# Kernel tuning notes

Measured on AMD Instinct MI355X. Metric: run time of the kernel, lower is better.

Reference implementation:

```python
import jax, jax.numpy as jnp
import numpy as np

EPS_LN = 1e-5
EPS_ATTN = 1e-8
NUM_ITER = 3

B, N, DIN = 64, 4096, 256
K, D, H = 8, 256, 512


def layer_norm(x, g, b):
    m = jnp.mean(x, axis=-1, keepdims=True)
    v = jnp.mean((x - m) ** 2, axis=-1, keepdims=True)
    return (x - m) * jax.lax.rsqrt(v + EPS_LN) * g + b


def gru_cell(x, h, W_ih, b_ih, W_hh, b_hh):
    # torch GRUCell: gates ordered (reset, update, new)
    gi = x @ W_ih.T + b_ih  # [BK, 3D]
    gh = h @ W_hh.T + b_hh
    ir, iz, inn = jnp.split(gi, 3, axis=-1)
    hr, hz, hn = jnp.split(gh, 3, axis=-1)
    r = jax.nn.sigmoid(ir + hr)
    z = jax.nn.sigmoid(iz + hz)
    n = jnp.tanh(inn + r * hn)
    return (1.0 - z) * n + z * h


def setup_inputs() -> dict:
    key = jax.random.key(0)
    ks = jax.random.split(key, 16)
    s = 1.0 / np.sqrt(D)
    si = 1.0 / np.sqrt(DIN)
    inp = {
        'inputs': jax.random.normal(ks[0], (B, N, DIN), jnp.float32),
        'noise': jax.random.normal(ks[1], (B, K, D), jnp.float32),
        'slot_mu': jax.random.normal(ks[2], (1, 1, D), jnp.float32),
        'slot_log_sigma': jnp.zeros((1, 1, D), jnp.float32),
        'Wq': jax.random.uniform(ks[3], (D, D), jnp.float32, -s, s),
        'bq': jnp.zeros((D,), jnp.float32),
        'Wk': jax.random.uniform(ks[4], (D, DIN), jnp.float32, -si, si),
        'bk': jnp.zeros((D,), jnp.float32),
        'Wv': jax.random.uniform(ks[5], (D, DIN), jnp.float32, -si, si),
        'bv': jnp.zeros((D,), jnp.float32),
        'W_ih': jax.random.uniform(ks[6], (3 * D, D), jnp.float32, -s, s),
        'b_ih': jnp.zeros((3 * D,), jnp.float32),
        'W_hh': jax.random.uniform(ks[7], (3 * D, D), jnp.float32, -s, s),
        'b_hh': jnp.zeros((3 * D,), jnp.float32),
        'ln_in_g': jnp.ones((DIN,), jnp.float32), 'ln_in_b': jnp.zeros((DIN,), jnp.float32),
        'ln_s_g': jnp.ones((D,), jnp.float32), 'ln_s_b': jnp.zeros((D,), jnp.float32),
        'ln_ff_g': jnp.ones((D,), jnp.float32), 'ln_ff_b': jnp.zeros((D,), jnp.float32),
        'W1': jax.random.uniform(ks[8], (H, D), jnp.float32, -s, s),
        'b1': jnp.zeros((H,), jnp.float32),
        'W2': jax.random.uniform(ks[9], (D, H), jnp.float32, -1.0 / np.sqrt(H), 1.0 / np.sqrt(H)),
        'b2': jnp.zeros((D,), jnp.float32),
    }
    return inp


def reference(inputs, noise, slot_mu, slot_log_sigma, Wq, bq, Wk, bk, Wv, bv,
              W_ih, b_ih, W_hh, b_hh, ln_in_g, ln_in_b, ln_s_g, ln_s_b,
              ln_ff_g, ln_ff_b, W1, b1, W2, b2):
    scale = D ** -0.5
    slots = slot_mu + jnp.exp(slot_log_sigma) * noise  # [B,K,D]
    x = layer_norm(inputs, ln_in_g, ln_in_b)
    k = x @ Wk.T + bk  # [B,N,D]
    v = x @ Wv.T + bv  # [B,N,D]
    attn = None
    for _ in range(NUM_ITER):
        slots_prev = slots
        sn = layer_norm(slots, ln_s_g, ln_s_b)
        q = sn @ Wq.T + bq  # [B,K,D]
        dots = jnp.einsum('bkd,bnd->bkn', q, k) * scale
        attn = jax.nn.softmax(dots, axis=1)  # softmax over slots
        attn_norm = attn / (jnp.sum(attn, axis=-1, keepdims=True) + EPS_ATTN)
        updates = jnp.einsum('bkn,bnd->bkd', attn_norm, v)
        h = gru_cell(updates.reshape(-1, D), slots_prev.reshape(-1, D),
                     W_ih, b_ih, W_hh, b_hh).reshape(slots.shape)
        ff = layer_norm(h, ln_ff_g, ln_ff_b)
        slots = h + (jax.nn.relu(ff @ W1.T + b1) @ W2.T + b2)
    return slots, attn
```

## Files before the change

### kernel.cpp

```cpp
#include <hip/hip_runtime.h>
#include <hip/hip_bf16.h>
#include <math.h>

typedef __bf16 bf16x8 __attribute__((ext_vector_type(8)));
typedef float f32x4 __attribute__((ext_vector_type(4)));

#define DEV static __device__ __forceinline__

DEV unsigned short f2b(float f){
  unsigned int u = __float_as_uint(f);
  u += 0x7fffu + ((u>>16)&1u);
  return (unsigned short)(u>>16);
}
DEV float b2f(unsigned short h){ return __uint_as_float(((unsigned int)h)<<16); }
DEV unsigned int pck(float a, float b){
  return (unsigned int)f2b(a) | ((unsigned int)f2b(b)<<16);
}
DEV f32x4 mfma16(bf16x8 a, bf16x8 b, f32x4 c){
  return __builtin_amdgcn_mfma_f32_16x16x32_bf16(a,b,c,0,0,0);
}
DEV float sigm(float x){ return 1.f/(1.f+expf(-x)); }

__global__ __launch_bounds__(256) void k_slots_init(
    const float* __restrict__ noise, const float* __restrict__ mu,
    const float* __restrict__ ls, float* __restrict__ sf,
    unsigned short* __restrict__ sb){
  int i = blockIdx.x*256 + threadIdx.x;
  int d = i & 255;
  float val = mu[d] + expf(ls[d]) * noise[i];
  sf[i] = val; sb[i] = f2b(val);
}

__global__ __launch_bounds__(256) void k_prep_b16(
    const float* __restrict__ Whh, const float* __restrict__ W1,
    const float* __restrict__ W2,
    unsigned short* __restrict__ Whhb, unsigned short* __restrict__ W1b,
    unsigned short* __restrict__ W2b){
  int i = blockIdx.x*256 + threadIdx.x;
  if (i < 196608) Whhb[i] = f2b(Whh[i]);
  else if (i < 327680) W1b[i-196608] = f2b(W1[i-196608]);
  else if (i < 458752) W2b[i-327680] = f2b(W2[i-327680]);
}

__global__ __launch_bounds__(256) void k_pre1(
    const float* __restrict__ Wq, const float* __restrict__ Wk,
    const float* __restrict__ bq, const float* __restrict__ bk,
    unsigned short* __restrict__ WcT, float* __restrict__ bc,
    float* __restrict__ wqbk, float* __restrict__ cbk){
  int c = blockIdx.x, d = threadIdx.x;
  float acc = 0.f;
  for (int e=0;e<256;e++)
    acc += Wq[e*256+d] * Wk[e*256+c];
  WcT[c*256+d] = f2b(acc);
  __shared__ float red[256];
  red[d] = bq[d] * Wk[d*256+c];
  __syncthreads();
  for (int s2=128;s2>0;s2>>=1){ if (d<s2) red[d]+=red[d+s2]; __syncthreads(); }
  if (d==0) bc[c] = red[0];
  if (blockIdx.x==0){
    float a2=0.f;
    for (int e=0;e<256;e++) a2 += Wq[e*256+d]*bk[e];
    wqbk[d] = a2;
    __syncthreads();
    red[d] = bq[d]*bk[d];
    __syncthreads();
    for (int s2=128;s2>0;s2>>=1){ if (d<s2) red[d]+=red[d+s2]; __syncthreads(); }
    if (d==0) cbk[0] = red[0];
  }
}

__global__ __launch_bounds__(256) void k_pre2(
    const float* __restrict__ W_ih, const float* __restrict__ Wv,
    const float* __restrict__ bv, const float* __restrict__ b_ih,
    unsigned short* __restrict__ WvihT, float* __restrict__ bvih){
  int j = blockIdx.x, c = threadIdx.x;
  float acc=0.f;
  for (int d=0; d<256; d++)
    acc += W_ih[j*256+d] * Wv[d*256+c];
  WvihT[j*256+c] = f2b(acc);
  __shared__ float red[256];
  red[c] = bv[c] * W_ih[j*256+c];
  __syncthreads();
  for (int s2=128;s2>0;s2>>=1){ if (c<s2) red[c]+=red[c+s2]; __syncthreads(); }
  if (c==0) bvih[j] = red[0] + b_ih[j];
}

__global__ __launch_bounds__(256) void k_slot_q(
    const float* __restrict__ sf, const float* __restrict__ g,
    const float* __restrict__ be,
    const unsigned short* __restrict__ WcT, const float* __restrict__ bc,
    const float* __restrict__ wqbk, const float* __restrict__ cbk,
    unsigned short* __restrict__ qp, float* __restrict__ dotbias,
    float* __restrict__ attn_sum){
  __shared__ __align__(16) unsigned short sn[16][264];
  int b = blockIdx.x, t = threadIdx.x;
  if (t < 8) attn_sum[b*8+t] = 0.f;
  if (t < 8) dotbias[b*16+8+t] = 0.f;
  int r = t>>5, j = t&31;
  const float* pr = sf + (b*8+r)*256 + j*8;
  float v[8]; float s=0.f;
  #pragma unroll
  for (int i=0;i<8;i++){ v[i]=pr[i]; s+=v[i]; }
  s += __shfl_xor(s,1); s+=__shfl_xor(s,2); s+=__shfl_xor(s,4);
  s += __shfl_xor(s,8); s+=__shfl_xor(s,16);
  float m = s*(1.f/256.f);
  float vs=0.f;
  #pragma unroll
  for (int i=0;i<8;i++){ float d = v[i]-m; vs += d*d; }
  vs += __shfl_xor(vs,1); vs+=__shfl_xor(vs,2); vs+=__shfl_xor(vs,4);
  vs += __shfl_xor(vs,8); vs+=__shfl_xor(vs,16);
  float rstd = rsqrtf(vs*(1.f/256.f) + 1e-5f);
  float dp = 0.f;
  #pragma unroll
  for (int i=0;i<8;i++){
    int d = j*8+i;
    float snv = (v[i]-m)*rstd*g[d] + be[d];
    sn[r][d] = f2b(snv);
    dp += snv * wqbk[d];
  }
  dp += __shfl_xor(dp,1); dp+=__shfl_xor(dp,2); dp+=__shfl_xor(dp,4);
  dp += __shfl_xor(dp,8); dp+=__shfl_xor(dp,16);
  if (j==0) dotbias[b*16+r] = dp + cbk[0];
  for (int rr=8; rr<16; ++rr){ sn[rr][t]=0; if (t<8) sn[rr][256+t]=0; }
  __syncthreads();
  int lane = t&63, wv = t>>6, l16 = lane&15, quad = lane>>4;
  #pragma unroll
  for (int nt=0; nt<4; ++nt){
    int col = (wv*4+nt)*16 + l16;
    f32x4 acc = {0.f,0.f,0.f,0.f};
    #pragma unroll
    for (int kk=0;kk<8;kk++){
      int kd = kk*32 + quad*8;
      bf16x8 a = *(const bf16x8*)&sn[l16][kd];
      bf16x8 bb = *(const bf16x8*)(WcT + col*256 + kd);
      acc = mfma16(a,bb,acc);
    }
    float bcv = bc[col];
    #pragma unroll
    for (int ri=0;ri<4;ri++){
      int rw = quad*4+ri;
      qp[(b*16+rw)*256 + col] = f2b(acc[ri] + bcv);
    }
  }
}

__global__ __launch_bounds__(256) void k_iter0(
    const float* __restrict__ in, const float* __restrict__ g,
    const float* __restrict__ be, const unsigned short* __restrict__ qp,
    const float* __restrict__ dotbias, float* __restrict__ attn_sum,
    float* __restrict__ upart, unsigned short* __restrict__ xc_w){
  __shared__ __align__(16) unsigned short xt[64][264];
  __shared__ __align__(16) float al[64][8];
  __shared__ float bsum[8];
  int t = threadIdx.x;
  int b = blockIdx.x >> 4, sp = blockIdx.x & 15;
  if (t<8) bsum[t]=0.f;
  int lane=t&63, wv=t>>6, l16=lane&15, quad=lane>>4;
  bf16x8 aq[8];
  #pragma unroll
  for (int kk=0;kk<8;kk++)
    aq[kk] = *(const bf16x8*)(qp + ((size_t)(b*16+l16))*256 + kk*32+quad*8);
  float db[4];
  #pragma unroll
  for (int ri=0;ri<4;ri++) db[ri] = dotbias[b*16 + quad*4 + ri];
  float acc8[8] = {0.f,0.f,0.f,0.f,0.f,0.f,0.f,0.f};
  int rl = t>>3, j = t&7;
  for (int tile=0; tile<4; ++tile){
    int n0 = sp*256 + tile*64;
    __syncthreads();
    #pragma unroll
    for (int p=0;p<2;p++){
      int row = p*32 + rl;
      const float* pr = in + ((size_t)(b*4096 + n0 + row))*256 + j*32;
      float v[32]; float s=0.f;
      #pragma unroll
      for (int c=0;c<8;c++) *(float4*)(v+c*4) = *(const float4*)(pr + c*4);
      #pragma unroll
      for (int i=0;i<32;i++) s += v[i];
      s += __shfl_xor(s,1); s+=__shfl_xor(s,2); s+=__shfl_xor(s,4);
      float m = s*(1.f/256.f);
      float vs=0.f;
      #pragma unroll
      for (int i=0;i<32;i++){ float d=v[i]-m; vs+=d*d; }
      vs+=__shfl_xor(vs,1); vs+=__shfl_xor(vs,2); vs+=__shfl_xor(vs,4);
      float rstd = rsqrtf(vs*(1.f/256.f)+1e-5f);
      #pragma unroll
      for (int c=0;c<4;c++){
        float o[8];
        #pragma unroll
        for (int q=0;q<8;q++){
          int d = j*32 + c*8 + q;
          o[q] = (v[c*8+q]-m)*rstd*g[d] + be[d];
        }
        uint4 w4;
        w4.x=pck(o[0],o[1]); w4.y=pck(o[2],o[3]);
        w4.z=pck(o[4],o[5]); w4.w=pck(o[6],o[7]);
        *(uint4*)&xt[row][j*32 + c*8] = w4;
        *(uint4*)(xc_w + ((size_t)(b*4096 + n0 + row))*256 + j*32 + c*8) = w4;
      }
    }
    __syncthreads();
    f32x4 acc = {0.f,0.f,0.f,0.f};
    #pragma unroll
    for (int kk=0;kk<8;kk++){
      int kd = kk*32 + quad*8;
      bf16x8 bb = *(const bf16x8*)&xt[wv*16 + l16][kd];
      acc = mfma16(aq[kk],bb,acc);
    }
    const float scale = 0.0625f;
    float val[4];
    #pragma unroll
    for (int ri=0;ri<4;ri++) val[ri] = (acc[ri] + db[ri]) * scale;
    float mx = fmaxf(fmaxf(val[0],val[1]), fmaxf(val[2],val[3]));
    mx = fmaxf(mx, __shfl_xor(mx,16));
    float e[4], s4=0.f;
    #pragma unroll
    for (int ri=0;ri<4;ri++){ e[ri] = expf(val[ri]-mx); s4 += e[ri]; }
    float s8 = s4 + __shfl_xor(s4,16);
    float inv = 1.f/s8;
    if (quad < 2){
      int nl = wv*16 + l16;
      #pragma unroll
      for (int ri=0;ri<4;ri++){
        float av = e[ri]*inv;
        int kr = quad*4+ri;
        al[nl][kr] = av;
        float ss = av;
        ss += __shfl_xor(ss,1); ss+=__shfl_xor(ss,2);
        ss += __shfl_xor(ss,4); ss+=__shfl_xor(ss,8);
        if (l16==0) atomicAdd(&bsum[kr], ss);
      }
    }
    __syncthreads();
    int c = t;
    #pragma unroll
    for (int n=0;n<64;++n){
      float xv = b2f(xt[n][c]);
      float4 a0 = *(const float4*)&al[n][0];
      float4 a1 = *(const float4*)&al[n][4];
      acc8[0]+=a0.x*xv; acc8[1]+=a0.y*xv; acc8[2]+=a0.z*xv; acc8[3]+=a0.w*xv;
      acc8[4]+=a1.x*xv; acc8[5]+=a1.y*xv; acc8[6]+=a1.z*xv; acc8[7]+=a1.w*xv;
    }
  }
  float* o = upart + (size_t)sp*131072 + ((size_t)b*8)*256 + t;
  #pragma unroll
  for (int k2=0;k2<8;k2++) o[(size_t)k2*256] = acc8[k2];
  if (t<8) atomicAdd(&attn_sum[b*8+t], bsum[t]);
}

__global__ __launch_bounds__(256) void k_iter(
    const unsigned short* __restrict__ xc,
    const unsigned short* __restrict__ qp,
    const float* __restrict__ dotbias, float* __restrict__ attn_sum,
    float* __restrict__ upart, float* __restrict__ attn_out){
  __shared__ __align__(16) unsigned short xt[64][264];
  __shared__ __align__(16) float al[64][8];
  __shared__ float bsum[8];
  int t = threadIdx.x;
  int b = blockIdx.x >> 4, sp = blockIdx.x & 15;
  if (t<8) bsum[t]=0.f;
  int lane=t&63, wv=t>>6, l16=lane&15, quad=lane>>4;
  bf16x8 aq[8];
  #pragma unroll
  for (int kk=0;kk<8;kk++)
    aq[kk] = *(const bf16x8*)(qp + ((size_t)(b*16+l16))*256 + kk*32+quad*8);
  float db[4];
  #pragma unroll
  for (int ri=0;ri<4;ri++) db[ri] = dotbias[b*16 + quad*4 + ri];
  float acc8[8] = {0.f,0.f,0.f,0.f,0.f,0.f,0.f,0.f};
  int rl = t>>3, j = t&7;
  const unsigned short* cbase = xc + ((size_t)(b*4096 + sp*256))*256;
  uint4 R[8];
  #pragma unroll
  for (int p=0;p<2;p++){
    const unsigned short* pr = cbase + (size_t)(p*32+rl)*256 + j*32;
    #pragma unroll
    for (int c=0;c<4;c++) R[p*4+c] = *(const uint4*)(pr + c*8);
  }
  for (int tile=0; tile<4; ++tile){
    #pragma unroll
    for (int p=0;p<2;p++){
      #pragma unroll
      for (int c=0;c<4;c++)
        *(uint4*)&xt[p*32+rl][j*32 + c*8] = R[p*4+c];
    }
    __syncthreads();
    if (tile<3){
      const unsigned short* nb = cbase + (size_t)(tile+1)*64*256;
      #pragma unroll
      for (int p=0;p<2;p++){
        const unsigned short* pr = nb + (size_t)(p*32+rl)*256 + j*32;
        #pragma unroll
        for (int c=0;c<4;c++) R[p*4+c] = *(const uint4*)(pr + c*8);
      }
    }
    int n0 = sp*256 + tile*64;
    f32x4 acc = {0.f,0.f,0.f,0.f};
    #pragma unroll
    for (int kk=0;kk<8;kk++){
      int kd = kk*32 + quad*8;
      bf16x8 bb = *(const bf16x8*)&xt[wv*16 + l16][kd];
      acc = mfma16(aq[kk],bb,acc);
    }
    const float scale = 0.0625f;
    float val[4];
    #pragma unroll
    for (int ri=0;ri<4;ri++) val[ri] = (acc[ri] + db[ri]) * scale;
    float mx = fmaxf(fmaxf(val[0],val[1]), fmaxf(val[2],val[3]));
    mx = fmaxf(mx, __shfl_xor(mx,16));
    float e[4], s4=0.f;
    #pragma unroll
    for (int ri=0;ri<4;ri++){ e[ri] = expf(val[ri]-mx); s4 += e[ri]; }
    float s8 = s4 + __shfl_xor(s4,16);
    float inv = 1.f/s8;
    if (quad < 2){
      int nl = wv*16 + l16;
      #pragma unroll
      for (int ri=0;ri<4;ri++){
        float av = e[ri]*inv;
        int kr = quad*4+ri;
        al[nl][kr] = av;
        if (attn_out)
          attn_out[((size_t)(b*8+kr))*4096 + n0 + nl] = av;
        float ss = av;
        ss += __shfl_xor(ss,1); ss+=__shfl_xor(ss,2);
        ss += __shfl_xor(ss,4); ss+=__shfl_xor(ss,8);
        if (l16==0) atomicAdd(&bsum[kr], ss);
      }
    }
    __syncthreads();
    int c = t;
    #pragma unroll
    for (int n=0;n<64;++n){
      float xv = b2f(xt[n][c]);
      float4 a0 = *(const float4*)&al[n][0];
      float4 a1 = *(const float4*)&al[n][4];
      acc8[0]+=a0.x*xv; acc8[1]+=a0.y*xv; acc8[2]+=a0.z*xv; acc8[3]+=a0.w*xv;
      acc8[4]+=a1.x*xv; acc8[5]+=a1.y*xv; acc8[6]+=a1.z*xv; acc8[7]+=a1.w*xv;
    }
    __syncthreads();
  }
  float* o = upart + (size_t)sp*131072 + ((size_t)b*8)*256 + t;
  #pragma unroll
  for (int k2=0;k2<8;k2++) o[(size_t)k2*256] = acc8[k2];
  if (t<8) atomicAdd(&attn_sum[b*8+t], bsum[t]);
}

__global__ __launch_bounds__(512) void k_step(
    const float* __restrict__ upart, float* __restrict__ asum,
    float* __restrict__ sf, unsigned short* __restrict__ sb,
    const unsigned short* __restrict__ WvihT, const float* __restrict__ bvih,
    const unsigned short* __restrict__ Whhb, const float* __restrict__ bhh,
    const float* __restrict__ lnffg, const float* __restrict__ lnffb,
    const unsigned short* __restrict__ W1b, const float* __restrict__ b1,
    const unsigned short* __restrict__ W2b, const float* __restrict__ b2v,
    const float* __restrict__ lnsg, const float* __restrict__ lnsb,
    const unsigned short* __restrict__ WcT, const float* __restrict__ bc,
    const float* __restrict__ wqbk, const float* __restrict__ cbk,
    unsigned short* __restrict__ qp, float* __restrict__ dotb,
    float* __restrict__ out_slots, int last){
  __shared__ __align__(16) unsigned short ub16[16][264];
  __shared__ __align__(16) float hls[16][268];
  __shared__ __align__(16) unsigned short sn[16][264];
  __shared__ __align__(16) unsigned short s1t[16][520];
  __shared__ float redh[8][16], redq[8][16], mr[16], rs[16];
  int t = threadIdx.x;
  int Bk = blockIdx.x;
  int bb0 = Bk*2;
  int lane=t&63, wv=t>>6, l16=lane&15, quad=lane>>4;
  {
    int r16 = t>>5, c0 = (t&31)*8;
    size_t base = ((size_t)(Bk*16 + r16))*256 + c0;
    float4 a0={0,0,0,0}, a1={0,0,0,0};
    #pragma unroll
    for (int sp2=0; sp2<16; ++sp2){
      const float* p = upart + (size_t)sp2*131072 + base;
      float4 u0=*(const float4*)(p+0), u1=*(const float4*)(p+4);
      a0.x+=u0.x;a0.y+=u0.y;a0.z+=u0.z;a0.w+=u0.w;
      a1.x+=u1.x;a1.y+=u1.y;a1.z+=u1.z;a1.w+=u1.w;
    }
    float inv = 1.f/(asum[Bk*16 + r16] + 1e-8f);
    float uu[8] = {a0.x,a0.y,a0.z,a0.w,a1.x,a1.y,a1.z,a1.w};
    #pragma unroll
    for (int c=0;c<8;c+=2)
      *(unsigned int*)&ub16[r16][c0+c] = pck(uu[c]*inv, uu[c+1]*inv);
  }
  __syncthreads();
  if (t < 16) asum[Bk*16 + t] = 0.f;
  bf16x8 afi[8], afh[8];
  #pragma unroll
  for (int kk=0;kk<8;kk++){
    int kd = kk*32+quad*8;
    afi[kk] = *(const bf16x8*)&ub16[l16][kd];
    afh[kk] = *(const bf16x8*)(sb + ((size_t)(Bk*16+l16))*256 + kd);
  }
  float sh[4]={0,0,0,0}, sq[4]={0,0,0,0};
  #pragma unroll
  for (int jj=0;jj<2;jj++){
    int jt = wv*2 + jj;
    int dR = jt*16 + l16;
    f32x4 cIR={0,0,0,0}, cIZ={0,0,0,0}, cIN={0,0,0,0};
    f32x4 cHR={0,0,0,0}, cHZ={0,0,0,0}, cHN={0,0,0,0};
    #pragma unroll
    for (int kk=0;kk<8;kk++){
      int kd = kk*32+quad*8;
      cIR = mfma16(afi[kk], *(const bf16x8*)(WvihT + (size_t)dR*256 + kd), cIR);
      cIZ = mfma16(afi[kk], *(const bf16x8*)(WvihT + (size_t)(256+dR)*256 + kd), cIZ);
      cIN = mfma16(afi[kk], *(const bf16x8*)(WvihT + (size_t)(512+dR)*256 + kd), cIN);
      cHR = mfma16(afh[kk], *(const bf16x8*)(Whhb + (size_t)dR*256 + kd), cHR);
      cHZ = mfma16(afh[kk], *(const bf16x8*)(Whhb + (size_t)(256+dR)*256 + kd), cHZ);
      cHN = mfma16(afh[kk], *(const bf16x8*)(Whhb + (size_t)(512+dR)*256 + kd), cHN);
    }
    float biR = bvih[dR], biZ = bvih[256+dR], biN = bvih[512+dR];
    float bhR = bhh[dR], bhZ = bhh[256+dR], bhN = bhh[512+dR];
    #pragma unroll
    for (int ri=0;ri<4;ri++){
      int row = quad*4+ri;
      float hp = sf[((size_t)(Bk*16+row))*256 + dR];
      float rg = sigm(cIR[ri]+biR + cHR[ri]+bhR);
      float z  = sigm(cIZ[ri]+biZ + cHZ[ri]+bhZ);
      float nn = tanhf(cIN[ri]+biN + rg*(cHN[ri]+bhN));
      float h = (1.f-z)*nn + z*hp;
      hls[row][dR] = h;
      sh[ri] += h; sq[ri] += h*h;
    }
  }
  #pragma unroll
  for (int ri=0;ri<4;ri++){
    sh[ri]+=__shfl_xor(sh[ri],1); sh[ri]+=__shfl_xor(sh[ri],2);
    sh[ri]+=__shfl_xor(sh[ri],4); sh[ri]+=__shfl_xor(sh[ri],8);
    sq[ri]+=__shfl_xor(sq[ri],1); sq[ri]+=__shfl_xor(sq[ri],2);
    sq[ri]+=__shfl_xor(sq[ri],4); sq[ri]+=__shfl_xor(sq[ri],8);
  }
  if (l16==0){
    #pragma unroll
    for (int ri=0;ri<4;ri++){
      redh[wv][quad*4+ri] = sh[ri];
      redq[wv][quad*4+ri] = sq[ri];
    }
  }
  __syncthreads();
  if (t < 16){
    float s = redh[0][t]+redh[1][t]+redh[2][t]+redh[3][t]
            + redh[4][t]+redh[5][t]+redh[6][t]+redh[7][t];
    float q = redq[0][t]+redq[1][t]+redq[2][t]+redq[3][t]
            + redq[4][t]+redq[5][t]+redq[6][t]+redq[7][t];
    float m = s*(1.f/256.f);
    float var = q*(1.f/256.f) - m*m;
    mr[t] = m; rs[t] = rsqrtf(var + 1e-5f);
  }
  __syncthreads();
  {
    int row = t>>5, c0 = (t&31)*8;
    float m = mr[row], rstd = rs[row];
    #pragma unroll
    for (int c=0;c<8;c+=2){
      int d = c0+c;
      float o0 = (hls[row][d]-m)*rstd*lnffg[d] + lnffb[d];
      float o1 = (hls[row][d+1]-m)*rstd*lnffg[d+1] + lnffb[d+1];
      *(unsigned int*)&sn[row][d] = pck(o0,o1);
    }
  }
  __syncthreads();
  {
    bf16x8 af[8];
    #pragma unroll
    for (int kk=0;kk<8;kk++)
      af[kk] = *(const bf16x8*)&sn[l16][kk*32+quad*8];
    #pragma unroll
    for (int ct=wv*4; ct<wv*4+4; ++ct){
      int col = ct*16+l16;
      f32x4 acc={0,0,0,0};
      #pragma unroll
      for (int kk=0;kk<8;kk++)
        acc = mfma16(af[kk], *(const bf16x8*)(W1b + (size_t)col*256 + kk*32+quad*8), acc);
      float bb = b1[col];
      #pragma unroll
      for (int ri=0;ri<4;ri++){
        float v2 = acc[ri]+bb; v2 = v2>0.f? v2:0.f;
        s1t[quad*4+ri][col] = f2b(v2);
      }
    }
  }
  __syncthreads();
  {
    bf16x8 af[16];
    #pragma unroll
    for (int kk=0;kk<16;kk++)
      af[kk] = *(const bf16x8*)&s1t[l16][kk*32+quad*8];
    #pragma unroll
    for (int ct=wv*2; ct<wv*2+2; ++ct){
      int col = ct*16+l16;
      f32x4 acc={0,0,0,0};
      #pragma unroll
      for (int kk=0;kk<16;kk++)
        acc = mfma16(af[kk], *(const bf16x8*)(W2b + (size_t)col*512 + kk*32+quad*8), acc);
      float bb = b2v[col];
      #pragma unroll
      for (int ri=0;ri<4;ri++){
        int row = quad*4+ri;
        float v2 = acc[ri] + bb + hls[row][col];
        size_t gidx = ((size_t)(Bk*16+row))*256 + col;
        sf[gidx] = v2;
        sb[gidx] = f2b(v2);
        if (last) out_slots[gidx] = v2;
        hls[row][col] = v2;
      }
    }
  }
  if (!last){
    __syncthreads();
    {
      int row = t>>5, c0 = (t&31)*8;
      float ps=0.f, pq=0.f;
      float hv[8];
      #pragma unroll
      for (int c=0;c<8;c++){ hv[c]=hls[row][c0+c]; ps+=hv[c]; pq+=hv[c]*hv[c]; }
      ps+=__shfl_xor(ps,1); ps+=__shfl_xor(ps,2); ps+=__shfl_xor(ps,4);
      ps+=__shfl_xor(ps,8); ps+=__shfl_xor(ps,16);
      pq+=__shfl_xor(pq,1); pq+=__shfl_xor(pq,2); pq+=__shfl_xor(pq,4);
      pq+=__shfl_xor(pq,8); pq+=__shfl_xor(pq,16);
      float m = ps*(1.f/256.f);
      float var = pq*(1.f/256.f) - m*m;
      float rstd = rsqrtf(var + 1e-5f);
      float dp = 0.f;
      #pragma unroll
      for (int c=0;c<8;c+=2){
        int d = c0+c;
        float o0 = (hv[c]-m)*rstd*lnsg[d] + lnsb[d];
        float o1 = (hv[c+1]-m)*rstd*lnsg[d+1] + lnsb[d+1];
        dp += o0*wqbk[d] + o1*wqbk[d+1];
        *(unsigned int*)&sn[row][d] = pck(o0,o1);
      }
      dp+=__shfl_xor(dp,1); dp+=__shfl_xor(dp,2); dp+=__shfl_xor(dp,4);
      dp+=__shfl_xor(dp,8); dp+=__shfl_xor(dp,16);
      if ((t&31)==0){
        int bloc = row>>3, rr = row&7;
        dotb[(bb0+bloc)*16 + rr] = dp + cbk[0];
      }
    }
    __syncthreads();
    {
      bf16x8 af[8];
      #pragma unroll
      for (int kk=0;kk<8;kk++)
        af[kk] = *(const bf16x8*)&sn[l16][kk*32+quad*8];
      #pragma unroll
      for (int ct=wv*2; ct<wv*2+2; ++ct){
        int col = ct*16+l16;
        f32x4 acc={0,0,0,0};
        #pragma unroll
        for (int kk=0;kk<8;kk++)
          acc = mfma16(af[kk], *(const bf16x8*)(WcT + (size_t)col*256 + kk*32+quad*8), acc);
        float bcv = bc[col];
        #pragma unroll
        for (int ri=0;ri<4;ri++){
          int row = quad*4+ri;
          int bloc = row>>3, rr = row&7;
          qp[((size_t)((bb0+bloc)*16 + rr))*256 + col] = f2b(acc[ri] + bcv);
        }
      }
    }
  }
}

extern "C" void kernel_launch(void* const* d_in, const int* in_sizes, int n_in,
                              void* d_out, int out_size, void* d_ws, size_t ws_size,
                              hipStream_t stream){
  const float* inputs  = (const float*)d_in[0];
  const float* noise   = (const float*)d_in[1];
  const float* slot_mu = (const float*)d_in[2];
  const float* slot_ls = (const float*)d_in[3];
  const float* Wq   = (const float*)d_in[4];
  const float* bq   = (const float*)d_in[5];
  const float* Wk   = (const float*)d_in[6];
  const float* bk   = (const float*)d_in[7];
  const float* Wv   = (const float*)d_in[8];
  const float* bv   = (const float*)d_in[9];
  const float* W_ih = (const float*)d_in[10];
  const float* b_ih = (const float*)d_in[11];
  const float* W_hh = (const float*)d_in[12];
  const float* b_hh = (const float*)d_in[13];
  const float* ln_in_g = (const float*)d_in[14];
  const float* ln_in_b = (const float*)d_in[15];
  const float* ln_s_g  = (const float*)d_in[16];
  const float* ln_s_b  = (const float*)d_in[17];
  const float* ln_ff_g = (const float*)d_in[18];
  const float* ln_ff_b = (const float*)d_in[19];
  const float* W1 = (const float*)d_in[20];
  const float* b1 = (const float*)d_in[21];
  const float* W2 = (const float*)d_in[22];
  const float* b2 = (const float*)d_in[23];

  char* w = (char*)d_ws;
  auto alloc = [&](size_t n)->char*{ char* p=w; w += (n+255)&~(size_t)255; return p; };
  unsigned short* xc   = (unsigned short*)alloc(134217728);
  float* upart         = (float*)alloc(8388608);
  unsigned short* qp   = (unsigned short*)alloc(524288);
  float* sf            = (float*)alloc(524288);
  unsigned short* sb   = (unsigned short*)alloc(262144);
  unsigned short* WcT  = (unsigned short*)alloc(131072);
  unsigned short* WvihT= (unsigned short*)alloc(393216);
  unsigned short* Whhb = (unsigned short*)alloc(393216);
  unsigned short* W1b  = (unsigned short*)alloc(262144);
  unsigned short* W2b  = (unsigned short*)alloc(262144);
  float* bc    = (float*)alloc(1024);
  float* wqbk  = (float*)alloc(1024);
  float* cbk   = (float*)alloc(256);
  float* bvih  = (float*)alloc(3072);
  float* dotb  = (float*)alloc(4096);
  float* asum  = (float*)alloc(2048);

  float* out_slots = (float*)d_out;
  float* out_attn  = out_slots + 131072;

  k_slots_init<<<dim3(512),dim3(256),0,stream>>>(noise, slot_mu, slot_ls, sf, sb);
  k_pre1<<<dim3(256),dim3(256),0,stream>>>(Wq, Wk, bq, bk, WcT, bc, wqbk, cbk);
  k_pre2<<<dim3(768),dim3(256),0,stream>>>(W_ih, Wv, bv, b_ih, WvihT, bvih);
  k_prep_b16<<<dim3(1792),dim3(256),0,stream>>>(W_hh, W1, W2, Whhb, W1b, W2b);
  k_slot_q<<<dim3(64),dim3(256),0,stream>>>(sf, ln_s_g, ln_s_b, WcT, bc, wqbk, cbk,
                                            qp, dotb, asum);

  for (int it=0; it<3; ++it){
    int last = (it==2);
    if (it==0){
      k_iter0<<<dim3(1024),dim3(256),0,stream>>>(
          inputs, ln_in_g, ln_in_b, qp, dotb, asum, upart, xc);
    } else {
      k_iter<<<dim3(1024),dim3(256),0,stream>>>(
          xc, qp, dotb, asum, upart,
          last ? out_attn : (float*)nullptr);
    }
    k_step<<<dim3(32),dim3(512),0,stream>>>(
        upart, asum, sf, sb, WvihT, bvih, Whhb, b_hh,
        ln_ff_g, ln_ff_b, W1b, b1, W2b, b2,
        ln_s_g, ln_s_b, WcT, bc, wqbk, cbk,
        qp, dotb, last ? out_slots : (float*)nullptr, last);
  }
}
```

Before: 799.7 us.

## Keep attention weights in registers via readlane and reduce updates per wave

The attention-weighted update accumulation no longer stages softmax weights in shared memory behind a block barrier. Each wave now broadcasts its own 16 tokens' weights with readlane and accumulates a partial 8x256 update over all 256 columns in registers. The four wave partials are summed through shared memory once at the end of the kernel, and per-slot attention sums are accumulated in registers before a single global atomic. This removes one barrier and the shared-memory weight traffic per tile, but uses more accumulator registers (32 floats per thread) and adds a cross-wave reduction step.

```diff
diff --git a/kernel.cpp b/kernel.cpp
--- a/kernel.cpp
+++ b/kernel.cpp
@@ -20,6 +20,7 @@
   return __builtin_amdgcn_mfma_f32_16x16x32_bf16(a,b,c,0,0,0);
 }
 DEV float sigm(float x){ return 1.f/(1.f+expf(-x)); }
+#define RDLANE(v, l) __uint_as_float(__builtin_amdgcn_readlane(__float_as_uint(v), (l)))
 
 __global__ __launch_bounds__(256) void k_slots_init(
     const float* __restrict__ noise, const float* __restrict__ mu,
@@ -150,11 +151,8 @@
     const float* __restrict__ dotbias, float* __restrict__ attn_sum,
     float* __restrict__ upart, unsigned short* __restrict__ xc_w){
   __shared__ __align__(16) unsigned short xt[64][264];
-  __shared__ __align__(16) float al[64][8];
-  __shared__ float bsum[8];
   int t = threadIdx.x;
   int b = blockIdx.x >> 4, sp = blockIdx.x & 15;
-  if (t<8) bsum[t]=0.f;
   int lane=t&63, wv=t>>6, l16=lane&15, quad=lane>>4;
   bf16x8 aq[8];
   #pragma unroll
@@ -163,7 +161,10 @@
   float db[4];
   #pragma unroll
   for (int ri=0;ri<4;ri++) db[ri] = dotbias[b*16 + quad*4 + ri];
-  float acc8[8] = {0.f,0.f,0.f,0.f,0.f,0.f,0.f,0.f};
+  float acc[8][4];
+  #pragma unroll
+  for (int k2=0;k2<8;k2++){ acc[k2][0]=0;acc[k2][1]=0;acc[k2][2]=0;acc[k2][3]=0; }
+  float rbs[4] = {0.f,0.f,0.f,0.f};
   int rl = t>>3, j = t&7;
   for (int tile=0; tile<4; ++tile){
     int n0 = sp*256 + tile*64;
@@ -200,17 +201,17 @@
       }
     }
     __syncthreads();
-    f32x4 acc = {0.f,0.f,0.f,0.f};
+    f32x4 dacc = {0.f,0.f,0.f,0.f};
     #pragma unroll
     for (int kk=0;kk<8;kk++){
       int kd = kk*32 + quad*8;
       bf16x8 bb = *(const bf16x8*)&xt[wv*16 + l16][kd];
-      acc = mfma16(aq[kk],bb,acc);
+      dacc = mfma16(aq[kk],bb,dacc);
     }
     const float scale = 0.0625f;
     float val[4];
     #pragma unroll
-    for (int ri=0;ri<4;ri++) val[ri] = (acc[ri] + db[ri]) * scale;
+    for (int ri=0;ri<4;ri++) val[ri] = (dacc[ri] + db[ri]) * scale;
     float mx = fmaxf(fmaxf(val[0],val[1]), fmaxf(val[2],val[3]));
     mx = fmaxf(mx, __shfl_xor(mx,16));
     float e[4], s4=0.f;
@@ -218,34 +219,56 @@
     for (int ri=0;ri<4;ri++){ e[ri] = expf(val[ri]-mx); s4 += e[ri]; }
     float s8 = s4 + __shfl_xor(s4,16);
     float inv = 1.f/s8;
+    float av[4];
+    #pragma unroll
+    for (int ri=0;ri<4;ri++) av[ri] = e[ri]*inv;
     if (quad < 2){
-      int nl = wv*16 + l16;
       #pragma unroll
       for (int ri=0;ri<4;ri++){
-        float av = e[ri]*inv;
-        int kr = quad*4+ri;
-        al[nl][kr] = av;
-        float ss = av;
+        float ss = av[ri];
         ss += __shfl_xor(ss,1); ss+=__shfl_xor(ss,2);
         ss += __shfl_xor(ss,4); ss+=__shfl_xor(ss,8);
-        if (l16==0) atomicAdd(&bsum[kr], ss);
-      }
-    }
-    __syncthreads();
-    int c = t;
-    #pragma unroll
-    for (int n=0;n<64;++n){
-      float xv = b2f(xt[n][c]);
-      float4 a0 = *(const float4*)&al[n][0];
-      float4 a1 = *(const float4*)&al[n][4];
-      acc8[0]+=a0.x*xv; acc8[1]+=a0.y*xv; acc8[2]+=a0.z*xv; acc8[3]+=a0.w*xv;
-      acc8[4]+=a1.x*xv; acc8[5]+=a1.y*xv; acc8[6]+=a1.z*xv; acc8[7]+=a1.w*xv;
-    }
-  }
+        if (l16==0) rbs[ri] += ss;
+      }
+    }
+    #pragma unroll
+    for (int nl=0; nl<16; ++nl){
+      int n = wv*16 + nl;
+      float xv0 = b2f(xt[n][lane]);
+      float xv1 = b2f(xt[n][64+lane]);
+      float xv2 = b2f(xt[n][128+lane]);
+      float xv3 = b2f(xt[n][192+lane]);
+      #pragma unroll
+      for (int ri=0;ri<4;ri++){
+        float alo = RDLANE(av[ri], nl);
+        float ahi = RDLANE(av[ri], nl+16);
+        acc[ri][0]   += alo*xv0; acc[ri][1]   += alo*xv1;
+        acc[ri][2]   += alo*xv2; acc[ri][3]   += alo*xv3;
+        acc[4+ri][0] += ahi*xv0; acc[4+ri][1] += ahi*xv1;
+        acc[4+ri][2] += ahi*xv2; acc[4+ri][3] += ahi*xv3;
+      }
+    }
+  }
+  __syncthreads();
+  float* ured = (float*)&xt[0][0];
+  #pragma unroll
+  for (int k2=0;k2<8;k2++)
+    #pragma unroll
+    for (int cc=0;cc<4;cc++)
+      ured[(wv*8+k2)*256 + cc*64 + lane] = acc[k2][cc];
+  __syncthreads();
   float* o = upart + (size_t)sp*131072 + ((size_t)b*8)*256 + t;
   #pragma unroll
-  for (int k2=0;k2<8;k2++) o[(size_t)k2*256] = acc8[k2];
-  if (t<8) atomicAdd(&attn_sum[b*8+t], bsum[t]);
+  for (int k2=0;k2<8;k2++){
+    float s = ured[k2*256+t] + ured[(8+k2)*256+t]
+            + ured[(16+k2)*256+t] + ured[(24+k2)*256+t];
+    o[(size_t)k2*256] = s;
+  }
+  if (quad < 2 && l16 == 0){
+    #pragma unroll
+    for (int ri=0;ri<4;ri++)
+      atomicAdd(&attn_sum[b*8 + quad*4 + ri], rbs[ri]);
+  }
 }
 
 __global__ __launch_bounds__(256) void k_iter(
@@ -254,11 +277,8 @@
     const float* __restrict__ dotbias, float* __restrict__ attn_sum,
     float* __restrict__ upart, float* __restrict__ attn_out){
   __shared__ __align__(16) unsigned short xt[64][264];
-  __shared__ __align__(16) float al[64][8];
-  __shared__ float bsum[8];
   int t = threadIdx.x;
   int b = blockIdx.x >> 4, sp = blockIdx.x & 15;
-  if (t<8) bsum[t]=0.f;
   int lane=t&63, wv=t>>6, l16=lane&15, quad=lane>>4;
   bf16x8 aq[8];
   #pragma unroll
@@ -267,7 +287,10 @@
   float db[4];
   #pragma unroll
   for (int ri=0;ri<4;ri++) db[ri] = dotbias[b*16 + quad*4 + ri];
-  float acc8[8] = {0.f,0.f,0.f,0.f,0.f,0.f,0.f,0.f};
+  float acc[8][4];
+  #pragma unroll
+  for (int k2=0;k2<8;k2++){ acc[k2][0]=0;acc[k2][1]=0;acc[k2][2]=0;acc[k2][3]=0; }
+  float rbs[4] = {0.f,0.f,0.f,0.f};
   int rl = t>>3, j = t&7;
   const unsigned short* cbase = xc + ((size_t)(b*4096 + sp*256))*256;
   uint4 R[8];
@@ -295,17 +318,17 @@
       }
     }
     int n0 = sp*256 + tile*64;
-    f32x4 acc = {0.f,0.f,0.f,0.f};
+    f32x4 dacc = {0.f,0.f,0.f,0.f};
     #pragma unroll
     for (int kk=0;kk<8;kk++){
       int kd = kk*32 + quad*8;
       bf16x8 bb = *(const bf16x8*)&xt[wv*16 + l16][kd];
-      acc = mfma16(aq[kk],bb,acc);
+      dacc = mfma16(aq[kk],bb,dacc);
     }
     const float scale = 0.0625f;
     float val[4];
     #pragma unroll
-    for (int ri=0;ri<4;ri++) val[ri] = (acc[ri] + db[ri]) * scale;
+    for (int ri=0;ri<4;ri++) val[ri] = (dacc[ri] + db[ri]) * scale;
     float mx = fmaxf(fmaxf(val[0],val[1]), fmaxf(val[2],val[3]));
     mx = fmaxf(mx, __shfl_xor(mx,16));
     float e[4], s4=0.f;
@@ -313,37 +336,60 @@
     for (int ri=0;ri<4;ri++){ e[ri] = expf(val[ri]-mx); s4 += e[ri]; }
     float s8 = s4 + __shfl_xor(s4,16);
     float inv = 1.f/s8;
+    float av[4];
+    #pragma unroll
+    for (int ri=0;ri<4;ri++) av[ri] = e[ri]*inv;
     if (quad < 2){
       int nl = wv*16 + l16;
       #pragma unroll
       for (int ri=0;ri<4;ri++){
-        float av = e[ri]*inv;
         int kr = quad*4+ri;
-        al[nl][kr] = av;
         if (attn_out)
-          attn_out[((size_t)(b*8+kr))*4096 + n0 + nl] = av;
-        float ss = av;
+          attn_out[((size_t)(b*8+kr))*4096 + n0 + nl] = av[ri];
+        float ss = av[ri];
         ss += __shfl_xor(ss,1); ss+=__shfl_xor(ss,2);
         ss += __shfl_xor(ss,4); ss+=__shfl_xor(ss,8);
-        if (l16==0) atomicAdd(&bsum[kr], ss);
-      }
-    }
-    __syncthreads();
-    int c = t;
-    #pragma unroll
-    for (int n=0;n<64;++n){
-      float xv = b2f(xt[n][c]);
-      float4 a0 = *(const float4*)&al[n][0];
-      float4 a1 = *(const float4*)&al[n][4];
-      acc8[0]+=a0.x*xv; acc8[1]+=a0.y*xv; acc8[2]+=a0.z*xv; acc8[3]+=a0.w*xv;
-      acc8[4]+=a1.x*xv; acc8[5]+=a1.y*xv; acc8[6]+=a1.z*xv; acc8[7]+=a1.w*xv;
-    }
-    __syncthreads();
-  }
+        if (l16==0) rbs[ri] += ss;
+      }
+    }
+    #pragma unroll
+    for (int nl=0; nl<16; ++nl){
+      int n = wv*16 + nl;
+      float xv0 = b2f(xt[n][lane]);
+      float xv1 = b2f(xt[n][64+lane]);
+      float xv2 = b2f(xt[n][128+lane]);
+      float xv3 = b2f(xt[n][192+lane]);
+      #pragma unroll
+      for (int ri=0;ri<4;ri++){
+        float alo = RDLANE(av[ri], nl);
+        float ahi = RDLANE(av[ri], nl+16);
+        acc[ri][0]   += alo*xv0; acc[ri][1]   += alo*xv1;
+        acc[ri][2]   += alo*xv2; acc[ri][3]   += alo*xv3;
+        acc[4+ri][0] += ahi*xv0; acc[4+ri][1] += ahi*xv1;
+        acc[4+ri][2] += ahi*xv2; acc[4+ri][3] += ahi*xv3;
+      }
+    }
+    __syncthreads();
+  }
+  float* ured = (float*)&xt[0][0];
+  #pragma unroll
+  for (int k2=0;k2<8;k2++)
+    #pragma unroll
+    for (int cc=0;cc<4;cc++)
+      ured[(wv*8+k2)*256 + cc*64 + lane] = acc[k2][cc];
+  __syncthreads();
   float* o = upart + (size_t)sp*131072 + ((size_t)b*8)*256 + t;
   #pragma unroll
-  for (int k2=0;k2<8;k2++) o[(size_t)k2*256] = acc8[k2];
-  if (t<8) atomicAdd(&attn_sum[b*8+t], bsum[t]);
+  for (int k2=0;k2<8;k2++){
+    float s = ured[k2*256+t] + ured[(8+k2)*256+t]
+            + ured[(16+k2)*256+t] + ured[(24+k2)*256+t];
+    o[(size_t)k2*256] = s;
+  }
+  if (quad < 2 && l16 == 0){
+    #pragma unroll
+    for (int ri=0;ri<4;ri++)
+      atomicAdd(&attn_sum[b*8 + quad*4 + ri], rbs[ri]);
+  }
 }
 
 __global__ __launch_bounds__(512) void k_step(
```

Measured after the change: 855.5 us. 1.07x slower.

## Broadcast attention weights via readlane, drop LDS atomics, widen step kernel to 1024 threads

Applied to the files above, without the earlier changes.

In the attention-update loops the per-token attention weights are now read once per lane from shared memory and broadcast with readlane, replacing two float4 LDS loads per token. Per-slot attention sums are kept in registers instead of going through shared-memory atomics. The small sequential step kernel goes from 512 to 1024 threads so each wave handles one column tile, spreading the GRU/MLP work across more waves. Readlane adds scalar-path instructions, and the larger block may raise register pressure or reduce the per-thread work below what the waves can hide.

```diff
diff --git a/kernel.cpp b/kernel.cpp
--- a/kernel.cpp
+++ b/kernel.cpp
@@ -20,6 +20,7 @@
   return __builtin_amdgcn_mfma_f32_16x16x32_bf16(a,b,c,0,0,0);
 }
 DEV float sigm(float x){ return 1.f/(1.f+expf(-x)); }
+#define RDLANE(v, l) __uint_as_float(__builtin_amdgcn_readlane(__float_as_uint(v), (l)))
 
 __global__ __launch_bounds__(256) void k_slots_init(
     const float* __restrict__ noise, const float* __restrict__ mu,
@@ -151,10 +152,8 @@
     float* __restrict__ upart, unsigned short* __restrict__ xc_w){
   __shared__ __align__(16) unsigned short xt[64][264];
   __shared__ __align__(16) float al[64][8];
-  __shared__ float bsum[8];
   int t = threadIdx.x;
   int b = blockIdx.x >> 4, sp = blockIdx.x & 15;
-  if (t<8) bsum[t]=0.f;
   int lane=t&63, wv=t>>6, l16=lane&15, quad=lane>>4;
   bf16x8 aq[8];
   #pragma unroll
@@ -164,6 +163,7 @@
   #pragma unroll
   for (int ri=0;ri<4;ri++) db[ri] = dotbias[b*16 + quad*4 + ri];
   float acc8[8] = {0.f,0.f,0.f,0.f,0.f,0.f,0.f,0.f};
+  float rbs[4] = {0.f,0.f,0.f,0.f};
   int rl = t>>3, j = t&7;
   for (int tile=0; tile<4; ++tile){
     int n0 = sp*256 + tile*64;
@@ -200,17 +200,17 @@
       }
     }
     __syncthreads();
-    f32x4 acc = {0.f,0.f,0.f,0.f};
+    f32x4 dacc = {0.f,0.f,0.f,0.f};
     #pragma unroll
     for (int kk=0;kk<8;kk++){
       int kd = kk*32 + quad*8;
       bf16x8 bb = *(const bf16x8*)&xt[wv*16 + l16][kd];
-      acc = mfma16(aq[kk],bb,acc);
+      dacc = mfma16(aq[kk],bb,dacc);
     }
     const float scale = 0.0625f;
     float val[4];
     #pragma unroll
-    for (int ri=0;ri<4;ri++) val[ri] = (acc[ri] + db[ri]) * scale;
+    for (int ri=0;ri<4;ri++) val[ri] = (dacc[ri] + db[ri]) * scale;
     float mx = fmaxf(fmaxf(val[0],val[1]), fmaxf(val[2],val[3]));
     mx = fmaxf(mx, __shfl_xor(mx,16));
     float e[4], s4=0.f;
@@ -218,34 +218,45 @@
     for (int ri=0;ri<4;ri++){ e[ri] = expf(val[ri]-mx); s4 += e[ri]; }
     float s8 = s4 + __shfl_xor(s4,16);
     float inv = 1.f/s8;
+    float av[4];
+    #pragma unroll
+    for (int ri=0;ri<4;ri++) av[ri] = e[ri]*inv;
     if (quad < 2){
       int nl = wv*16 + l16;
       #pragma unroll
       for (int ri=0;ri<4;ri++){
-        float av = e[ri]*inv;
-        int kr = quad*4+ri;
-        al[nl][kr] = av;
-        float ss = av;
+        al[nl][quad*4+ri] = av[ri];
+        float ss = av[ri];
         ss += __shfl_xor(ss,1); ss+=__shfl_xor(ss,2);
         ss += __shfl_xor(ss,4); ss+=__shfl_xor(ss,8);
-        if (l16==0) atomicAdd(&bsum[kr], ss);
+        if (l16==0) rbs[ri] += ss;
       }
     }
     __syncthreads();
-    int c = t;
+    float areg[8];
+    *(float4*)&areg[0] = *(const float4*)&al[lane][0];
+    *(float4*)&areg[4] = *(const float4*)&al[lane][4];
     #pragma unroll
     for (int n=0;n<64;++n){
-      float xv = b2f(xt[n][c]);
-      float4 a0 = *(const float4*)&al[n][0];
-      float4 a1 = *(const float4*)&al[n][4];
-      acc8[0]+=a0.x*xv; acc8[1]+=a0.y*xv; acc8[2]+=a0.z*xv; acc8[3]+=a0.w*xv;
-      acc8[4]+=a1.x*xv; acc8[5]+=a1.y*xv; acc8[6]+=a1.z*xv; acc8[7]+=a1.w*xv;
+      float xv = b2f(xt[n][t]);
+      acc8[0] += RDLANE(areg[0], n) * xv;
+      acc8[1] += RDLANE(areg[1], n) * xv;
+      acc8[2] += RDLANE(areg[2], n) * xv;
+      acc8[3] += RDLANE(areg[3], n) * xv;
+      acc8[4] += RDLANE(areg[4], n) * xv;
+      acc8[5] += RDLANE(areg[5], n) * xv;
+      acc8[6] += RDLANE(areg[6], n) * xv;
+      acc8[7] += RDLANE(areg[7], n) * xv;
     }
   }
   float* o = upart + (size_t)sp*131072 + ((size_t)b*8)*256 + t;
   #pragma unroll
   for (int k2=0;k2<8;k2++) o[(size_t)k2*256] = acc8[k2];
-  if (t<8) atomicAdd(&attn_sum[b*8+t], bsum[t]);
+  if (quad < 2 && l16 == 0){
+    #pragma unroll
+    for (int ri=0;ri<4;ri++)
+      atomicAdd(&attn_sum[b*8 + quad*4 + ri], rbs[ri]);
+  }
 }
 
 __global__ __launch_bounds__(256) void k_iter(
@@ -255,10 +266,8 @@
     float* __restrict__ upart, float* __restrict__ attn_out){
   __shared__ __align__(16) unsigned short xt[64][264];
   __shared__ __align__(16) float al[64][8];
-  __shared__ float bsum[8];
   int t = threadIdx.x;
   int b = blockIdx.x >> 4, sp = blockIdx.x & 15;
-  if (t<8) bsum[t]=0.f;
   int lane=t&63, wv=t>>6, l16=lane&15, quad=lane>>4;
   bf16x8 aq[8];
   #pragma unroll
@@ -268,6 +277,7 @@
   #pragma unroll
   for (int ri=0;ri<4;ri++) db[ri] = dotbias[b*16 + quad*4 + ri];
   float acc8[8] = {0.f,0.f,0.f,0.f,0.f,0.f,0.f,0.f};
+  float rbs[4] = {0.f,0.f,0.f,0.f};
   int rl = t>>3, j = t&7;
   const unsigned short* cbase = xc + ((size_t)(b*4096 + sp*256))*256;
   uint4 R[8];
@@ -295,17 +305,17 @@
       }
     }
     int n0 = sp*256 + tile*64;
-    f32x4 acc = {0.f,0.f,0.f,0.f};
+    f32x4 dacc = {0.f,0.f,0.f,0.f};
     #pragma unroll
     for (int kk=0;kk<8;kk++){
       int kd = kk*32 + quad*8;
       bf16x8 bb = *(const bf16x8*)&xt[wv*16 + l16][kd];
-      acc = mfma16(aq[kk],bb,acc);
+      dacc = mfma16(aq[kk],bb,dacc);
     }
     const float scale = 0.0625f;
     float val[4];
     #pragma unroll
-    for (int ri=0;ri<4;ri++) val[ri] = (acc[ri] + db[ri]) * scale;
+    for (int ri=0;ri<4;ri++) val[ri] = (dacc[ri] + db[ri]) * scale;
     float mx = fmaxf(fmaxf(val[0],val[1]), fmaxf(val[2],val[3]));
     mx = fmaxf(mx, __shfl_xor(mx,16));
     float e[4], s4=0.f;
@@ -313,40 +323,52 @@
     for (int ri=0;ri<4;ri++){ e[ri] = expf(val[ri]-mx); s4 += e[ri]; }
     float s8 = s4 + __shfl_xor(s4,16);
     float inv = 1.f/s8;
+    float av[4];
+    #pragma unroll
+    for (int ri=0;ri<4;ri++) av[ri] = e[ri]*inv;
     if (quad < 2){
       int nl = wv*16 + l16;
       #pragma unroll
       for (int ri=0;ri<4;ri++){
-        float av = e[ri]*inv;
         int kr = quad*4+ri;
-        al[nl][kr] = av;
+        al[nl][kr] = av[ri];
         if (attn_out)
-          attn_out[((size_t)(b*8+kr))*4096 + n0 + nl] = av;
-        float ss = av;
+          attn_out[((size_t)(b*8+kr))*4096 + n0 + nl] = av[ri];
+        float ss = av[ri];
         ss += __shfl_xor(ss,1); ss+=__shfl_xor(ss,2);
         ss += __shfl_xor(ss,4); ss+=__shfl_xor(ss,8);
-        if (l16==0) atomicAdd(&bsum[kr], ss);
+        if (l16==0) rbs[ri] += ss;
       }
     }
     __syncthreads();
-    int c = t;
+    float areg[8];
+    *(float4*)&areg[0] = *(const float4*)&al[lane][0];
+    *(float4*)&areg[4] = *(const float4*)&al[lane][4];
     #pragma unroll
     for (int n=0;n<64;++n){
-      float xv = b2f(xt[n][c]);
-      float4 a0 = *(const float4*)&al[n][0];
-      float4 a1 = *(const float4*)&al[n][4];
-      acc8[0]+=a0.x*xv; acc8[1]+=a0.y*xv; acc8[2]+=a0.z*xv; acc8[3]+=a0.w*xv;
-      acc8[4]+=a1.x*xv; acc8[5]+=a1.y*xv; acc8[6]+=a1.z*xv; acc8[7]+=a1.w*xv;
+      float xv = b2f(xt[n][t]);
+      acc8[0] += RDLANE(areg[0], n) * xv;
+      acc8[1] += RDLANE(areg[1], n) * xv;
+      acc8[2] += RDLANE(areg[2], n) * xv;
+      acc8[3] += RDLANE(areg[3], n) * xv;
+      acc8[4] += RDLANE(areg[4], n) * xv;
+      acc8[5] += RDLANE(areg[5], n) * xv;
+      acc8[6] += RDLANE(areg[6], n) * xv;
+      acc8[7] += RDLANE(areg[7], n) * xv;
     }
     __syncthreads();
   }
   float* o = upart + (size_t)sp*131072 + ((size_t)b*8)*256 + t;
   #pragma unroll
   for (int k2=0;k2<8;k2++) o[(size_t)k2*256] = acc8[k2];
-  if (t<8) atomicAdd(&attn_sum[b*8+t], bsum[t]);
-}
-
-__global__ __launch_bounds__(512) void k_step(
+  if (quad < 2 && l16 == 0){
+    #pragma unroll
+    for (int ri=0;ri<4;ri++)
+      atomicAdd(&attn_sum[b*8 + quad*4 + ri], rbs[ri]);
+  }
+}
+
+__global__ __launch_bounds__(1024) void k_step(
     const float* __restrict__ upart, float* __restrict__ asum,
     float* __restrict__ sf, unsigned short* __restrict__ sb,
     const unsigned short* __restrict__ WvihT, const float* __restrict__ bvih,
@@ -363,27 +385,24 @@
   __shared__ __align__(16) float hls[16][268];
   __shared__ __align__(16) unsigned short sn[16][264];
   __shared__ __align__(16) unsigned short s1t[16][520];
-  __shared__ float redh[8][16], redq[8][16], mr[16], rs[16];
+  __shared__ float redh[16][16], redq[16][16], mr[16], rs[16];
   int t = threadIdx.x;
   int Bk = blockIdx.x;
   int bb0 = Bk*2;
   int lane=t&63, wv=t>>6, l16=lane&15, quad=lane>>4;
   {
-    int r16 = t>>5, c0 = (t&31)*8;
+    int r16 = t>>6, c0 = (t&63)*4;
     size_t base = ((size_t)(Bk*16 + r16))*256 + c0;
-    float4 a0={0,0,0,0}, a1={0,0,0,0};
+    float4 a0={0,0,0,0};
     #pragma unroll
     for (int sp2=0; sp2<16; ++sp2){
       const float* p = upart + (size_t)sp2*131072 + base;
-      float4 u0=*(const float4*)(p+0), u1=*(const float4*)(p+4);
+      float4 u0=*(const float4*)p;
       a0.x+=u0.x;a0.y+=u0.y;a0.z+=u0.z;a0.w+=u0.w;
-      a1.x+=u1.x;a1.y+=u1.y;a1.z+=u1.z;a1.w+=u1.w;
     }
     float inv = 1.f/(asum[Bk*16 + r16] + 1e-8f);
-    float uu[8] = {a0.x,a0.y,a0.z,a0.w,a1.x,a1.y,a1.z,a1.w};
-    #pragma unroll
-    for (int c=0;c<8;c+=2)
-      *(unsigned int*)&ub16[r16][c0+c] = pck(uu[c]*inv, uu[c+1]*inv);
+    *(unsigned int*)&ub16[r16][c0]   = pck(a0.x*inv, a0.y*inv);
+    *(unsigned int*)&ub16[r16][c0+2] = pck(a0.z*inv, a0.w*inv);
   }
   __syncthreads();
   if (t < 16) asum[Bk*16 + t] = 0.f;
@@ -395,10 +414,8 @@
     afh[kk] = *(const bf16x8*)(sb + ((size_t)(Bk*16+l16))*256 + kd);
   }
   float sh[4]={0,0,0,0}, sq[4]={0,0,0,0};
-  #pragma unroll
-  for (int jj=0;jj<2;jj++){
-    int jt = wv*2 + jj;
-    int dR = jt*16 + l16;
+  {
+    int dR = wv*16 + l16;
     f32x4 cIR={0,0,0,0}, cIZ={0,0,0,0}, cIN={0,0,0,0};
     f32x4 cHR={0,0,0,0}, cHZ={0,0,0,0}, cHN={0,0,0,0};
     #pragma unroll
@@ -441,25 +458,23 @@
   }
   __syncthreads();
   if (t < 16){
-    float s = redh[0][t]+redh[1][t]+redh[2][t]+redh[3][t]
-            + redh[4][t]+redh[5][t]+redh[6][t]+redh[7][t];
-    float q = redq[0][t]+redq[1][t]+redq[2][t]+redq[3][t]
-            + redq[4][t]+redq[5][t]+redq[6][t]+redq[7][t];
+    float s = 0.f, q = 0.f;
+    #pragma unroll
+    for (int w2=0;w2<16;w2++){ s += redh[w2][t]; q += redq[w2][t]; }
     float m = s*(1.f/256.f);
     float var = q*(1.f/256.f) - m*m;
     mr[t] = m; rs[t] = rsqrtf(var + 1e-5f);
   }
   __syncthreads();
   {
-    int row = t>>5, c0 = (t&31)*8;
+    int row = t>>6, c0 = (t&63)*4;
     float m = mr[row], rstd = rs[row];
-    #pragma unroll
-    for (int c=0;c<8;c+=2){
-      int d = c0+c;
-      float o0 = (hls[row][d]-m)*rstd*lnffg[d] + lnffb[d];
-      float o1 = (hls[row][d+1]-m)*rstd*lnffg[d+1] + lnffb[d+1];
-      *(unsigned int*)&sn[row][d] = pck(o0,o1);
-    }
+    float o0 = (hls[row][c0+0]-m)*rstd*lnffg[c0+0] + lnffb[c0+0];
+    float o1 = (hls[row][c0+1]-m)*rstd*lnffg[c0+1] + lnffb[c0+1];
+    float o2 = (hls[row][c0+2]-m)*rstd*lnffg[c0+2] + lnffb[c0+2];
+    float o3 = (hls[row][c0+3]-m)*rstd*lnffg[c0+3] + lnffb[c0+3];
+    *(unsigned int*)&sn[row][c0]   = pck(o0,o1);
+    *(unsigned int*)&sn[row][c0+2] = pck(o2,o3);
   }
   __syncthreads();
   {
@@ -468,7 +483,7 @@
     for (int kk=0;kk<8;kk++)
       af[kk] = *(const bf16x8*)&sn[l16][kk*32+quad*8];
     #pragma unroll
-    for (int ct=wv*4; ct<wv*4+4; ++ct){
+    for (int ct=wv*2; ct<wv*2+2; ++ct){
       int col = ct*16+l16;
       f32x4 acc={0,0,0,0};
       #pragma unroll
@@ -488,53 +503,49 @@
     #pragma unroll
     for (int kk=0;kk<16;kk++)
       af[kk] = *(const bf16x8*)&s1t[l16][kk*32+quad*8];
-    #pragma unroll
-    for (int ct=wv*2; ct<wv*2+2; ++ct){
-      int col = ct*16+l16;
-      f32x4 acc={0,0,0,0};
-      #pragma unroll
-      for (int kk=0;kk<16;kk++)
-        acc = mfma16(af[kk], *(const bf16x8*)(W2b + (size_t)col*512 + kk*32+quad*8), acc);
-      float bb = b2v[col];
-      #pragma unroll
-      for (int ri=0;ri<4;ri++){
-        int row = quad*4+ri;
-        float v2 = acc[ri] + bb + hls[row][col];
-        size_t gidx = ((size_t)(Bk*16+row))*256 + col;
-        sf[gidx] = v2;
-        sb[gidx] = f2b(v2);
-        if (last) out_slots[gidx] = v2;
-        hls[row][col] = v2;
-      }
+    int col = wv*16+l16;
+    f32x4 acc={0,0,0,0};
+    #pragma unroll
+    for (int kk=0;kk<16;kk++)
+      acc = mfma16(af[kk], *(const bf16x8*)(W2b + (size_t)col*512 + kk*32+quad*8), acc);
+    float bb = b2v[col];
+    #pragma unroll
+    for (int ri=0;ri<4;ri++){
+      int row = quad*4+ri;
+      float v2 = acc[ri] + bb + hls[row][col];
+      size_t gidx = ((size_t)(Bk*16+row))*256 + col;
+      sf[gidx] = v2;
+      sb[gidx] = f2b(v2);
+      if (last) out_slots[gidx] = v2;
+      hls[row][col] = v2;
     }
   }
   if (!last){
     __syncthreads();
     {
-      int row = t>>5, c0 = (t&31)*8;
+      int row = t>>6, c0 = (t&63)*4;
+      float hv[4];
       float ps=0.f, pq=0.f;
-      float hv[8];
-      #pragma unroll
-      for (int c=0;c<8;c++){ hv[c]=hls[row][c0+c]; ps+=hv[c]; pq+=hv[c]*hv[c]; }
+      #pragma unroll
+      for (int c=0;c<4;c++){ hv[c]=hls[row][c0+c]; ps+=hv[c]; pq+=hv[c]*hv[c]; }
       ps+=__shfl_xor(ps,1); ps+=__shfl_xor(ps,2); ps+=__shfl_xor(ps,4);
-      ps+=__shfl_xor(ps,8); ps+=__shfl_xor(ps,16);
+      ps+=__shfl_xor(ps,8); ps+=__shfl_xor(ps,16); ps+=__shfl_xor(ps,32);
       pq+=__shfl_xor(pq,1); pq+=__shfl_xor(pq,2); pq+=__shfl_xor(pq,4);
-      pq+=__shfl_xor(pq,8); pq+=__shfl_xor(pq,16);
+      pq+=__shfl_xor(pq,8); pq+=__shfl_xor(pq,16); pq+=__shfl_xor(pq,32);
       float m = ps*(1.f/256.f);
       float var = pq*(1.f/256.f) - m*m;
       float rstd = rsqrtf(var + 1e-5f);
       float dp = 0.f;
-      #pragma unroll
-      for (int c=0;c<8;c+=2){
-        int d = c0+c;
-        float o0 = (hv[c]-m)*rstd*lnsg[d] + lnsb[d];
-        float o1 = (hv[c+1]-m)*rstd*lnsg[d+1] + lnsb[d+1];
-        dp += o0*wqbk[d] + o1*wqbk[d+1];
-        *(unsigned int*)&sn[row][d] = pck(o0,o1);
-      }
+      float o0 = (hv[0]-m)*rstd*lnsg[c0+0] + lnsb[c0+0];
+      float o1 = (hv[1]-m)*rstd*lnsg[c0+1] + lnsb[c0+1];
+      float o2 = (hv[2]-m)*rstd*lnsg[c0+2] + lnsb[c0+2];
+      float o3 = (hv[3]-m)*rstd*lnsg[c0+3] + lnsb[c0+3];
+      dp += o0*wqbk[c0+0] + o1*wqbk[c0+1] + o2*wqbk[c0+2] + o3*wqbk[c0+3];
+      *(unsigned int*)&sn[row][c0]   = pck(o0,o1);
+      *(unsigned int*)&sn[row][c0+2] = pck(o2,o3);
       dp+=__shfl_xor(dp,1); dp+=__shfl_xor(dp,2); dp+=__shfl_xor(dp,4);
-      dp+=__shfl_xor(dp,8); dp+=__shfl_xor(dp,16);
-      if ((t&31)==0){
+      dp+=__shfl_xor(dp,8); dp+=__shfl_xor(dp,16); dp+=__shfl_xor(dp,32);
+      if ((t&63)==0){
         int bloc = row>>3, rr = row&7;
         dotb[(bb0+bloc)*16 + rr] = dp + cbk[0];
       }
@@ -545,20 +556,17 @@
       #pragma unroll
       for (int kk=0;kk<8;kk++)
         af[kk] = *(const bf16x8*)&sn[l16][kk*32+quad*8];
-      #pragma unroll
-      for (int ct=wv*2; ct<wv*2+2; ++ct){
-        int col = ct*16+l16;
-        f32x4 acc={0,0,0,0};
-        #pragma unroll
-        for (int kk=0;kk<8;kk++)
-          acc = mfma16(af[kk], *(const bf16x8*)(WcT + (size_t)col*256 + kk*32+quad*8), acc);
-        float bcv = bc[col];
-        #pragma unroll
-        for (int ri=0;ri<4;ri++){
-          int row = quad*4+ri;
-          int bloc = row>>3, rr = row&7;
-          qp[((size_t)((bb0+bloc)*16 + rr))*256 + col] = f2b(acc[ri] + bcv);
-        }
+      int col = wv*16+l16;
+      f32x4 acc={0,0,0,0};
+      #pragma unroll
+      for (int kk=0;kk<8;kk++)
+        acc = mfma16(af[kk], *(const bf16x8*)(WcT + (size_t)col*256 + kk*32+quad*8), acc);
+      float bcv = bc[col];
+      #pragma unroll
+      for (int ri=0;ri<4;ri++){
+        int row = quad*4+ri;
+        int bloc = row>>3, rr = row&7;
+        qp[((size_t)((bb0+bloc)*16 + rr))*256 + col] = f2b(acc[ri] + bcv);
       }
     }
   }
@@ -631,7 +639,7 @@
           xc, qp, dotb, asum, upart,
           last ? out_attn : (float*)nullptr);
     }
-    k_step<<<dim3(32),dim3(512),0,stream>>>(
+    k_step<<<dim3(32),dim3(1024),0,stream>>>(
         upart, asum, sf, sb, WvihT, bvih, Whhb, b_hh,
         ln_ff_g, ln_ff_b, W1b, b1, W2b, b2,
         ln_s_g, ln_s_b, WcT, bc, wqbk, cbk,
```

Result: slower. 841.7 us (+5.3%).
